# Kernel optimization log

Hardware: AMD Instinct MI355X
Metric: run time of the kernel (lower is better)

Reference implementation:

```python
import jax, jax.numpy as jnp
import numpy as np
import math

LATENT_D = 64
NDIM = 2
VEC = LATENT_D // 4          # 16 output rows per hyper-generated weight
D_LAT = 64                   # channels-proj input dim (latent last dim)
POSENC_CH = 31               # nerf posenc: 1 + 2*15 per coordinate
CH = [NDIM * POSENC_CH, VEC, VEC, VEC]  # [62, 16, 16, 16]
N_PTS = 32768
BATCH = 16
LN_EPS = 1e-5


def posenc_nerf(x, min_deg=0, max_deg=15):
    # x: [..., D] -> [..., D*(1 + 2*(max_deg-min_deg))]
    scales = 2.0 ** jnp.arange(min_deg, max_deg, dtype=x.dtype)
    xb = (x[..., None, :] * scales[:, None]).reshape(*x.shape[:-1], -1)
    emb = jnp.sin(jnp.concatenate([xb, xb + jnp.pi / 2.0], axis=-1))
    return jnp.concatenate([x, emb], axis=-1)


def layernorm(h, w, b):
    mu = h.mean(-1, keepdims=True)
    var = ((h - mu) ** 2).mean(-1, keepdims=True)
    return (h - mu) / jnp.sqrt(var + LN_EPS) * w + b


def setup_inputs() -> dict:
    key = jax.random.key(0)
    ks = iter(jax.random.split(key, 40))
    inp = {}
    inp["x"] = jax.random.uniform(next(ks), (N_PTS, NDIM), dtype=jnp.float32)
    inp["latent"] = jax.random.normal(next(ks), (BATCH, LATENT_D, D_LAT), dtype=jnp.float32)
    for i, ch in enumerate(CH):
        s = 1.0 / math.sqrt(D_LAT)
        inp[f"pw{i}"] = jax.random.normal(next(ks), (VEC * ch, D_LAT), dtype=jnp.float32) * s
        inp[f"pb{i}"] = jax.random.normal(next(ks), (VEC * ch,), dtype=jnp.float32) * 0.01
        inp[f"lnw{i}"] = jnp.full((ch,), 0.0625, dtype=jnp.float32)  # learned_scale init
        inp[f"lnb{i}"] = jnp.zeros((ch,), dtype=jnp.float32)
        inp[f"mb{i}"] = jax.random.normal(next(ks), (VEC,), dtype=jnp.float32)  # registered bias (randn init)
    dims = [(100, VEC), (100, 100), (1, 100)]
    for j, (o, i_) in enumerate(dims, 1):
        s = 1.0 / math.sqrt(i_)
        inp[f"w{j}"] = jax.random.uniform(next(ks), (o, i_), dtype=jnp.float32, minval=-s, maxval=s)
        inp[f"b{j}"] = jax.random.uniform(next(ks), (o,), dtype=jnp.float32, minval=-s, maxval=s)
    return inp


def reference(x, latent,
              pw0, pb0, lnw0, lnb0, mb0,
              pw1, pb1, lnw1, lnb1, mb1,
              pw2, pb2, lnw2, lnb2, mb2,
              pw3, pb3, lnw3, lnb3, mb3,
              w1, b1, w2, b2, w3, b3):
    B = latent.shape[0]
    # x[None].repeat(B,1,1) then nerf-encode: [B, N, 62]
    h = posenc_nerf(jnp.broadcast_to(x[None], (B,) + x.shape))
    proj = [(pw0, pb0, lnw0, lnb0, mb0), (pw1, pb1, lnw1, lnb1, mb1),
            (pw2, pb2, lnw2, lnb2, mb2), (pw3, pb3, lnw3, lnb3, mb3)]
    start = 0
    for (pw, pb, lnw, lnb, mb), ch in zip(proj, CH):
        lat = latent[:, start:start + VEC, :]           # [B, 16, 64]
        start += VEC
        # ChannelsProj: einsum + LN(channels) + bias -> per-sample weight [B, 16, ch]
        wv = jnp.einsum('bvd,vcd->bvc', lat, pw.reshape(VEC, ch, D_LAT))
        wv = layernorm(wv, lnw, lnb) + pb.reshape(VEC, ch)
        # hyper-MLP stage: bmm + bias + SiLU
        h = jax.nn.silu(jnp.einsum('bpi,boi->bpo', h, wv) + mb)
    # trailing dense MLP: 16 -> 100 -> 100 -> 1
    h = jax.nn.silu(h @ w1.T + b1)
    h = jax.nn.silu(h @ w2.T + b2)
    h = h @ w3.T + b3
    return h.squeeze(-1)  # [B, N]
```

## Files before the change

kernel.cpp:

```cpp
#include <hip/hip_runtime.h>

#define N_PTS 32768
#define BATCH 16
#define PIO2F 1.5707963705062866f

typedef __attribute__((ext_vector_type(8))) _Float16 half8;
typedef __attribute__((ext_vector_type(4))) _Float16 half4;
typedef __attribute__((ext_vector_type(4))) float f32x4;

__device__ __forceinline__ float silu_f(float v) {
    return v * __builtin_amdgcn_rcpf(1.0f + __expf(-v));
}

__device__ __forceinline__ float wave_sum(float v) {
    #pragma unroll
    for (int off = 1; off < 64; off <<= 1) v += __shfl_xor(v, off, 64);
    return v;
}

__device__ __forceinline__ void lds_fence() {
    asm volatile("" ::: "memory");
#if __has_builtin(__builtin_amdgcn_wave_barrier)
    __builtin_amdgcn_wave_barrier();
#else
    __builtin_amdgcn_sched_barrier(0);
#endif
    asm volatile("" ::: "memory");
}

__device__ __forceinline__ f32x4 mfma16h(half8 a, half8 b, f32x4 c) {
    return __builtin_amdgcn_mfma_f32_16x16x32_f16(a, b, c, 0, 0, 0);
}

__device__ __forceinline__ half8 h8zero() {
    half8 z;
    #pragma unroll
    for (int r = 0; r < 8; ++r) z[r] = (_Float16)0.0f;
    return z;
}

__device__ __forceinline__ half8 xlane_frag(f32x4 acc, int s0b, int s1b) {
    union { _Float16 h[4]; int i[2]; } p;
    #pragma unroll
    for (int r = 0; r < 4; ++r) p.h[r] = (_Float16)silu_f(acc[r]);
    union { int i[4]; half8 v; } o;
    o.i[0] = __builtin_amdgcn_ds_bpermute(s0b, p.i[0]);
    o.i[1] = __builtin_amdgcn_ds_bpermute(s0b, p.i[1]);
    o.i[2] = __builtin_amdgcn_ds_bpermute(s1b, p.i[0]);
    o.i[3] = __builtin_amdgcn_ds_bpermute(s1b, p.i[1]);
    return o.v;
}

__global__ void wv_kernel(
    const float* __restrict__ latent,
    const float* __restrict__ pw0, const float* __restrict__ pb0,
    const float* __restrict__ lnw0, const float* __restrict__ lnb0,
    const float* __restrict__ pw1, const float* __restrict__ pb1,
    const float* __restrict__ lnw1, const float* __restrict__ lnb1,
    const float* __restrict__ pw2, const float* __restrict__ pb2,
    const float* __restrict__ lnw2, const float* __restrict__ lnb2,
    const float* __restrict__ pw3, const float* __restrict__ pb3,
    const float* __restrict__ lnw3, const float* __restrict__ lnb3,
    float* __restrict__ wvb) {
    int blk = blockIdx.x;
    int l = blk >> 8;
    int rest = blk & 255;
    int b = rest >> 4, o = rest & 15;
    int c = threadIdx.x;

    const float *pw, *pb, *lnw, *lnb;
    float* outp;
    int ch;
    switch (l) {
        case 0:  pw = pw0; pb = pb0; lnw = lnw0; lnb = lnb0; outp = wvb;                 ch = 62; break;
        case 1:  pw = pw1; pb = pb1; lnw = lnw1; lnb = lnb1; outp = wvb + 15872;         ch = 16; break;
        case 2:  pw = pw2; pb = pb2; lnw = lnw2; lnb = lnb2; outp = wvb + 15872 + 4096;  ch = 16; break;
        default: pw = pw3; pb = pb3; lnw = lnw3; lnb = lnb3; outp = wvb + 15872 + 8192;  ch = 16; break;
    }
    const float* lat = latent + ((size_t)(b * 64 + l * 16 + o)) * 64;
    float dot = 0.f;
    if (c < ch) {
        const float* pr = pw + ((size_t)(o * ch + c)) * 64;
        #pragma unroll
        for (int d0 = 0; d0 < 64; d0++) dot += lat[d0] * pr[d0];
    }
    float act = (c < ch) ? dot : 0.f;
    float mu = wave_sum(act) * (1.0f / ch);
    float diff = (c < ch) ? (dot - mu) : 0.f;
    float var = wave_sum(diff * diff) * (1.0f / ch);
    float norm = diff * rsqrtf(var + 1e-5f);
    if (c < ch) outp[(size_t)(b * 16 + o) * ch + c] = norm * lnw[c] + lnb[c] + pb[o * ch + c];
}

__global__ __launch_bounds__(256) void posenc_pre(
    const float* __restrict__ xg, _Float16* __restrict__ peh) {
    int p = blockIdx.x * 256 + threadIdx.x;
    float x0 = xg[2 * p], x1 = xg[2 * p + 1];
    size_t pbs = (size_t)(p >> 4) * 1024 + (size_t)(p & 15) * 8;
    #pragma unroll
    for (int c = 0; c < 8; ++c) {
        half8 hv;
        #pragma unroll
        for (int j = 0; j < 8; ++j) {
            float v;
            if (c < 4) {
                int f = 8 * c + j;
                int idx2 = f - 2;
                int s = idx2 >> 1;
                float sc = __uint_as_float((unsigned)(127 + s) << 23);
                float xa = (idx2 & 1) ? x1 : x0;
                v = sinf(xa * sc);
                if (f == 0) v = x0;
                if (f == 1) v = x1;
            } else {
                int t = 8 * (c - 4) + j;
                int s = t >> 1;
                float sc = __uint_as_float((unsigned)(127 + s) << 23);
                float xa = (t & 1) ? x1 : x0;
                v = sinf(fmaf(xa, sc, PIO2F));
                if (t >= 30) v = 0.f;
            }
            hv[j] = (_Float16)v;
        }
        *(half8*)(peh + pbs + c * 128) = hv;
    }
}

#define BOUNCE_OFF  0
#define W2H_OFF     20480
#define W1H_OFF     41280
#define WV0H_OFF    46656
#define WVH_OFF     48960
#define B1_OFF      51264
#define B2_OFF      51712
#define W3_OFF      52160
#define MB_LDS_OFF  52608
#define LDS_TOTAL   52864

template <bool PRE>
__global__ __launch_bounds__(512, 2) void mfma_kernel(
    const float* __restrict__ xg,
    const _Float16* __restrict__ peh,
    const float* __restrict__ wvb,
    const float* __restrict__ mb0, const float* __restrict__ mb1,
    const float* __restrict__ mb2, const float* __restrict__ mb3,
    const float* __restrict__ w1, const float* __restrict__ b1,
    const float* __restrict__ w2, const float* __restrict__ b2,
    const float* __restrict__ w3, const float* __restrict__ b3,
    float* __restrict__ out) {
    extern __shared__ char smem[];
    _Float16* lds_bounce = (_Float16*)(smem + BOUNCE_OFF);
    _Float16* lds_w2h    = (_Float16*)(smem + W2H_OFF);
    _Float16* lds_w1h    = (_Float16*)(smem + W1H_OFF);
    _Float16* lds_wv0h   = (_Float16*)(smem + WV0H_OFF);
    _Float16* lds_wvh    = (_Float16*)(smem + WVH_OFF);
    float*    lds_b1     = (float*)(smem + B1_OFF);
    float*    lds_b2     = (float*)(smem + B2_OFF);
    float*    lds_w3     = (float*)(smem + W3_OFF);
    float*    lds_mb     = (float*)(smem + MB_LDS_OFF);

    const int b  = blockIdx.x >> 6;
    const int p0 = (blockIdx.x & 63) * 512;

    for (int idx = threadIdx.x; idx < 100 * 104; idx += 512) {
        int o = idx / 104, k = idx - o * 104;
        lds_w2h[idx] = (_Float16)((k < 100) ? w2[o * 100 + k] : 0.f);
    }
    for (int idx = threadIdx.x; idx < 112 * 24; idx += 512) {
        int o = idx / 24, k = idx - o * 24;
        lds_w1h[idx] = (_Float16)((o < 100 && k < 16) ? w1[o * 16 + k] : 0.f);
    }
    const float* wv0g = wvb + b * 992;
    for (int idx = threadIdx.x; idx < 16 * 72; idx += 512) {
        int o = idx / 72, k = idx - o * 72;
        lds_wv0h[idx] = (_Float16)((k < 62) ? wv0g[o * 62 + k] : 0.f);
    }
    const float* wv1g = wvb + 15872 + b * 256;
    const float* wv2g = wvb + 15872 + 4096 + b * 256;
    const float* wv3g = wvb + 15872 + 8192 + b * 256;
    for (int idx = threadIdx.x; idx < 3 * 16 * 24; idx += 512) {
        int li = idx / 384, rest = idx - li * 384;
        int o = rest / 24, k = rest - o * 24;
        const float* src = (li == 0) ? wv1g : (li == 1) ? wv2g : wv3g;
        lds_wvh[idx] = (_Float16)((k < 16) ? src[o * 16 + k] : 0.f);
    }
    if (threadIdx.x < 112) {
        int o = threadIdx.x;
        lds_b1[o] = (o < 100) ? b1[o] : 0.f;
        lds_b2[o] = (o < 100) ? b2[o] : 0.f;
        lds_w3[o] = (o < 100) ? w3[o] : 0.f;
    }
    if (threadIdx.x >= 128 && threadIdx.x < 192) {
        int t = threadIdx.x - 128;
        int li = t >> 4, o = t & 15;
        const float* mbp = (li == 0) ? mb0 : (li == 1) ? mb1 : (li == 2) ? mb2 : mb3;
        lds_mb[t] = mbp[o];
    }
    __syncthreads();

    const int l    = threadIdx.x & 63;
    const int w    = threadIdx.x >> 6;
    const int lrow = l & 15;
    const int lkg  = l >> 4;
    _Float16* bwA = lds_bounce + w * 1280;
    _Float16* bwB = bwA + 640;
    const int pbase = w * 64;
    const float b3v = b3[0];
    const int ptg0 = (p0 + pbase) >> 4;
    const bool kmask = (lkg >= 2);
    const int s0b = (lrow + 32 * (lkg & 1)) * 4;
    const int s1b = s0b + 64;

    #pragma unroll 1
    for (int it = 0; it < 2; ++it) {
        const int ptA = it * 2;
        const int pcolA = p0 + pbase + ptA * 16 + lrow;
        const int pcolB = pcolA + 16;

        half8 pb0A, pb1A, pb0B, pb1B;
        if (PRE) {
            size_t baseA = (size_t)(ptg0 + ptA) * 1024 + (size_t)lkg * 128 + (size_t)lrow * 8;
            pb0A = *(const half8*)(peh + baseA);
            pb1A = *(const half8*)(peh + baseA + 512);
            pb0B = *(const half8*)(peh + baseA + 1024);
            pb1B = *(const half8*)(peh + baseA + 1536);
        } else {
            #pragma unroll
            for (int ch = 0; ch < 2; ++ch) {
                const int pc = ch ? pcolB : pcolA;
                const float x0 = xg[2 * pc], x1 = xg[2 * pc + 1];
                half8 t0, t1;
                #pragma unroll
                for (int j = 0; j < 8; ++j) {
                    int idx2 = 8 * lkg + j - 2;
                    int s = idx2 >> 1;
                    float sc = __uint_as_float((unsigned)(127 + s) << 23);
                    float xa = (idx2 & 1) ? x1 : x0;
                    float v = sinf(xa * sc);
                    if (lkg == 0 && j == 0) v = x0;
                    if (lkg == 0 && j == 1) v = x1;
                    t0[j] = (_Float16)v;
                }
                #pragma unroll
                for (int j = 0; j < 8; ++j) {
                    int t = 8 * lkg + j;
                    int s = t >> 1;
                    float sc = __uint_as_float((unsigned)(127 + s) << 23);
                    float xa = (t & 1) ? x1 : x0;
                    float v = sinf(fmaf(xa, sc, PIO2F));
                    if (t >= 30) v = 0.f;
                    t1[j] = (_Float16)v;
                }
                if (ch) { pb0B = t0; pb1B = t1; } else { pb0A = t0; pb1A = t1; }
            }
        }

        f32x4 accA = *(const f32x4*)(lds_mb + lkg * 4);
        f32x4 accB = accA;
        {
            half8 a0 = *(const half8*)(lds_wv0h + lrow * 72 + lkg * 8);
            accA = mfma16h(a0, pb0A, accA);
            accB = mfma16h(a0, pb0B, accB);
            a0 = *(const half8*)(lds_wv0h + lrow * 72 + 32 + lkg * 8);
            accA = mfma16h(a0, pb1A, accA);
            accB = mfma16h(a0, pb1B, accB);
        }

        #pragma unroll
        for (int li = 0; li < 3; ++li) {
            half8 fA = xlane_frag(accA, s0b, s1b);
            half8 fB = xlane_frag(accB, s0b, s1b);
            f32x4 bias = *(const f32x4*)(lds_mb + (li + 1) * 16 + lkg * 4);
            half8 ah = *(const half8*)(lds_wvh + (li * 16 + lrow) * 24 + (lkg & 1) * 8);
            if (kmask) ah = h8zero();
            accA = mfma16h(ah, fA, bias);
            accB = mfma16h(ah, fB, bias);
        }
        half8 hbfA = xlane_frag(accA, s0b, s1b);
        half8 hbfB = xlane_frag(accB, s0b, s1b);

        f32x4 a2A[7], a2B[7];
        #pragma unroll
        for (int f2 = 0; f2 < 7; ++f2) {
            f32x4 bias = *(const f32x4*)(lds_b2 + f2 * 16 + lkg * 4);
            a2A[f2] = bias;
            a2B[f2] = bias;
        }
        #pragma unroll
        for (int ks = 0; ks < 4; ++ks) {
            lds_fence();
            #pragma unroll
            for (int lf = 0; lf < 2; ++lf) {
                const int fmt = 2 * ks + lf;
                if (fmt < 7) {
                    f32x4 bias = *(const f32x4*)(lds_b1 + fmt * 16 + lkg * 4);
                    half8 ah = *(const half8*)(lds_w1h + (fmt * 16 + lrow) * 24 + (lkg & 1) * 8);
                    if (kmask) ah = h8zero();
                    f32x4 a1A = mfma16h(ah, hbfA, bias);
                    f32x4 a1B = mfma16h(ah, hbfB, bias);
                    half4 hvA, hvB;
                    #pragma unroll
                    for (int r = 0; r < 4; ++r) {
                        hvA[r] = (_Float16)silu_f(a1A[r]);
                        hvB[r] = (_Float16)silu_f(a1B[r]);
                    }
                    *(half4*)(bwA + lrow * 40 + lf * 16 + lkg * 4) = hvA;
                    *(half4*)(bwB + lrow * 40 + lf * 16 + lkg * 4) = hvB;
                } else {
                    half4 hz;
                    #pragma unroll
                    for (int r = 0; r < 4; ++r) hz[r] = (_Float16)0.0f;
                    *(half4*)(bwA + lrow * 40 + lf * 16 + lkg * 4) = hz;
                    *(half4*)(bwB + lrow * 40 + lf * 16 + lkg * 4) = hz;
                }
            }
            lds_fence();
            half8 h2fA = *(const half8*)(bwA + lrow * 40 + lkg * 8);
            half8 h2fB = *(const half8*)(bwB + lrow * 40 + lkg * 8);
            const int kb = ks * 32 + lkg * 8;
            const int kba = (ks == 3) ? ((kb > 96) ? 96 : kb) : kb;
            __builtin_amdgcn_s_setprio(1);
            #pragma unroll
            for (int f2 = 0; f2 < 7; ++f2) {
                int arow = f2 * 16 + lrow;
                if (f2 == 6) arow = (arow > 99) ? 99 : arow;
                half8 ah = *(const half8*)(lds_w2h + arow * 104 + kba);
                a2A[f2] = mfma16h(ah, h2fA, a2A[f2]);
                a2B[f2] = mfma16h(ah, h2fB, a2B[f2]);
            }
            __builtin_amdgcn_s_setprio(0);
        }

        float outA = 0.f, outB = 0.f;
        #pragma unroll
        for (int f2 = 0; f2 < 7; ++f2) {
            f32x4 w3v = *(const f32x4*)(lds_w3 + f2 * 16 + lkg * 4);
            #pragma unroll
            for (int r = 0; r < 4; ++r) {
                outA = fmaf(silu_f(a2A[f2][r]), w3v[r], outA);
                outB = fmaf(silu_f(a2B[f2][r]), w3v[r], outB);
            }
        }
        outA += __shfl_xor(outA, 16, 64);
        outA += __shfl_xor(outA, 32, 64);
        outB += __shfl_xor(outB, 16, 64);
        outB += __shfl_xor(outB, 32, 64);
        if (l < 16) {
            out[(size_t)b * N_PTS + pcolA] = outA + b3v;
            out[(size_t)b * N_PTS + pcolB] = outB + b3v;
        }
    }
}

extern "C" void kernel_launch(void* const* d_in, const int* in_sizes, int n_in,
                              void* d_out, int out_size, void* d_ws, size_t ws_size,
                              hipStream_t stream) {
    const float* x = (const float*)d_in[0];
    const float* latent = (const float*)d_in[1];
    const float *pw[4], *pb[4], *lnw[4], *lnb[4], *mb[4];
    for (int l = 0; l < 4; l++) {
        pw[l]  = (const float*)d_in[2 + 5 * l];
        pb[l]  = (const float*)d_in[3 + 5 * l];
        lnw[l] = (const float*)d_in[4 + 5 * l];
        lnb[l] = (const float*)d_in[5 + 5 * l];
        mb[l]  = (const float*)d_in[6 + 5 * l];
    }
    const float* w1 = (const float*)d_in[22];
    const float* b1 = (const float*)d_in[23];
    const float* w2 = (const float*)d_in[24];
    const float* b2 = (const float*)d_in[25];
    const float* w3 = (const float*)d_in[26];
    const float* b3 = (const float*)d_in[27];

    float* wvb = (float*)d_ws;
    _Float16* peh = (_Float16*)((char*)d_ws + 112640);
    const size_t WS_NEED = 112640 + (size_t)N_PTS * 64 * sizeof(_Float16);
    bool pre = ws_size >= WS_NEED;

    wv_kernel<<<1024, 64, 0, stream>>>(latent,
        pw[0], pb[0], lnw[0], lnb[0],
        pw[1], pb[1], lnw[1], lnb[1],
        pw[2], pb[2], lnw[2], lnb[2],
        pw[3], pb[3], lnw[3], lnb[3],
        wvb);

    if (pre) {
        posenc_pre<<<N_PTS / 256, 256, 0, stream>>>(x, peh);
        hipFuncSetAttribute((const void*)mfma_kernel<true>,
                            hipFuncAttributeMaxDynamicSharedMemorySize, LDS_TOTAL);
        mfma_kernel<true><<<BATCH * (N_PTS / 512), 512, LDS_TOTAL, stream>>>(
            x, peh, wvb, mb[0], mb[1], mb[2], mb[3],
            w1, b1, w2, b2, w3, b3, (float*)d_out);
    } else {
        hipFuncSetAttribute((const void*)mfma_kernel<false>,
                            hipFuncAttributeMaxDynamicSharedMemorySize, LDS_TOTAL);
        mfma_kernel<false><<<BATCH * (N_PTS / 512), 512, LDS_TOTAL, stream>>>(
            x, peh, wvb, mb[0], mb[1], mb[2], mb[3],
            w1, b1, w2, b2, w3, b3, (float*)d_out);
    }
}
```

Before: 75.09 us.

## Replace LDS bounce buffer with register bpermute for layer-1 to layer-2 fragments

Layer-1 MFMA outputs are now all computed up front, passed through SiLU, packed to fp16 in registers, and moved into the B-operand layout for layer 2 with ds_bpermute and a lane-mask select. This replaces the per-wave LDS bounce buffer, its write/read round trips and the wave fences. It also drops the setprio hints. Removing the 20 KB bounce region cuts LDS use, which may allow more blocks per CU, but holding 28 packed ints live raises register pressure under the 512x2 launch bounds.

```diff
diff --git a/kernel.cpp b/kernel.cpp
--- a/kernel.cpp
+++ b/kernel.cpp
@@ -18,16 +18,6 @@
     return v;
 }
 
-__device__ __forceinline__ void lds_fence() {
-    asm volatile("" ::: "memory");
-#if __has_builtin(__builtin_amdgcn_wave_barrier)
-    __builtin_amdgcn_wave_barrier();
-#else
-    __builtin_amdgcn_sched_barrier(0);
-#endif
-    asm volatile("" ::: "memory");
-}
-
 __device__ __forceinline__ f32x4 mfma16h(half8 a, half8 b, f32x4 c) {
     return __builtin_amdgcn_mfma_f32_16x16x32_f16(a, b, c, 0, 0, 0);
 }
@@ -39,15 +29,33 @@
     return z;
 }
 
+__device__ __forceinline__ void silu_pack(f32x4 acc, int& d0, int& d1) {
+    union { _Float16 h[4]; int i[2]; } p;
+    #pragma unroll
+    for (int r = 0; r < 4; ++r) p.h[r] = (_Float16)silu_f(acc[r]);
+    d0 = p.i[0]; d1 = p.i[1];
+}
+
+__device__ __forceinline__ half8 bperm_frag(int d0, int d1, int s0b, int s1b) {
+    union { int i[4]; half8 v; } o;
+    o.i[0] = __builtin_amdgcn_ds_bpermute(s0b, d0);
+    o.i[1] = __builtin_amdgcn_ds_bpermute(s0b, d1);
+    o.i[2] = __builtin_amdgcn_ds_bpermute(s1b, d0);
+    o.i[3] = __builtin_amdgcn_ds_bpermute(s1b, d1);
+    return o.v;
+}
+
 __device__ __forceinline__ half8 xlane_frag(f32x4 acc, int s0b, int s1b) {
-    union { _Float16 h[4]; int i[2]; } p;
-    #pragma unroll
-    for (int r = 0; r < 4; ++r) p.h[r] = (_Float16)silu_f(acc[r]);
-    union { int i[4]; half8 v; } o;
-    o.i[0] = __builtin_amdgcn_ds_bpermute(s0b, p.i[0]);
-    o.i[1] = __builtin_amdgcn_ds_bpermute(s0b, p.i[1]);
-    o.i[2] = __builtin_amdgcn_ds_bpermute(s1b, p.i[0]);
-    o.i[3] = __builtin_amdgcn_ds_bpermute(s1b, p.i[1]);
+    int d0, d1;
+    silu_pack(acc, d0, d1);
+    return bperm_frag(d0, d1, s0b, s1b);
+}
+
+__device__ __forceinline__ half8 sel_frag(bool m, half8 a, half8 b) {
+    union { half8 v; int i[4]; } ua, ub, o;
+    ua.v = a; ub.v = b;
+    #pragma unroll
+    for (int r = 0; r < 4; ++r) o.i[r] = m ? ua.i[r] : ub.i[r];
     return o.v;
 }
 
@@ -126,16 +134,15 @@
     }
 }
 
-#define BOUNCE_OFF  0
-#define W2H_OFF     20480
-#define W1H_OFF     41280
-#define WV0H_OFF    46656
-#define WVH_OFF     48960
-#define B1_OFF      51264
-#define B2_OFF      51712
-#define W3_OFF      52160
-#define MB_LDS_OFF  52608
-#define LDS_TOTAL   52864
+#define W2H_OFF     0
+#define W1H_OFF     20800
+#define WV0H_OFF    26176
+#define WVH_OFF     28480
+#define B1_OFF      30784
+#define B2_OFF      31232
+#define W3_OFF      31680
+#define MB_LDS_OFF  32128
+#define LDS_TOTAL   32384
 
 template <bool PRE>
 __global__ __launch_bounds__(512, 2) void mfma_kernel(
@@ -149,7 +156,6 @@
     const float* __restrict__ w3, const float* __restrict__ b3,
     float* __restrict__ out) {
     extern __shared__ char smem[];
-    _Float16* lds_bounce = (_Float16*)(smem + BOUNCE_OFF);
     _Float16* lds_w2h    = (_Float16*)(smem + W2H_OFF);
     _Float16* lds_w1h    = (_Float16*)(smem + W1H_OFF);
     _Float16* lds_wv0h   = (_Float16*)(smem + WV0H_OFF);
@@ -202,8 +208,6 @@
     const int w    = threadIdx.x >> 6;
     const int lrow = l & 15;
     const int lkg  = l >> 4;
-    _Float16* bwA = lds_bounce + w * 1280;
-    _Float16* bwB = bwA + 640;
     const int pbase = w * 64;
     const float b3v = b3[0];
     const int ptg0 = (p0 + pbase) >> 4;
@@ -279,6 +283,18 @@
         half8 hbfA = xlane_frag(accA, s0b, s1b);
         half8 hbfB = xlane_frag(accB, s0b, s1b);
 
+        int a1A[14], a1B[14];
+        #pragma unroll
+        for (int fmt = 0; fmt < 7; ++fmt) {
+            f32x4 bias = *(const f32x4*)(lds_b1 + fmt * 16 + lkg * 4);
+            half8 ah = *(const half8*)(lds_w1h + (fmt * 16 + lrow) * 24 + (lkg & 1) * 8);
+            if (kmask) ah = h8zero();
+            f32x4 vA = mfma16h(ah, hbfA, bias);
+            f32x4 vB = mfma16h(ah, hbfB, bias);
+            silu_pack(vA, a1A[2 * fmt], a1A[2 * fmt + 1]);
+            silu_pack(vB, a1B[2 * fmt], a1B[2 * fmt + 1]);
+        }
+
         f32x4 a2A[7], a2B[7];
         #pragma unroll
         for (int f2 = 0; f2 < 7; ++f2) {
@@ -288,38 +304,16 @@
         }
         #pragma unroll
         for (int ks = 0; ks < 4; ++ks) {
-            lds_fence();
-            #pragma unroll
-            for (int lf = 0; lf < 2; ++lf) {
-                const int fmt = 2 * ks + lf;
-                if (fmt < 7) {
-                    f32x4 bias = *(const f32x4*)(lds_b1 + fmt * 16 + lkg * 4);
-                    half8 ah = *(const half8*)(lds_w1h + (fmt * 16 + lrow) * 24 + (lkg & 1) * 8);
-                    if (kmask) ah = h8zero();
-                    f32x4 a1A = mfma16h(ah, hbfA, bias);
-                    f32x4 a1B = mfma16h(ah, hbfB, bias);
-                    half4 hvA, hvB;
-                    #pragma unroll
-                    for (int r = 0; r < 4; ++r) {
-                        hvA[r] = (_Float16)silu_f(a1A[r]);
-                        hvB[r] = (_Float16)silu_f(a1B[r]);
-                    }
-                    *(half4*)(bwA + lrow * 40 + lf * 16 + lkg * 4) = hvA;
-                    *(half4*)(bwB + lrow * 40 + lf * 16 + lkg * 4) = hvB;
-                } else {
-                    half4 hz;
-                    #pragma unroll
-                    for (int r = 0; r < 4; ++r) hz[r] = (_Float16)0.0f;
-                    *(half4*)(bwA + lrow * 40 + lf * 16 + lkg * 4) = hz;
-                    *(half4*)(bwB + lrow * 40 + lf * 16 + lkg * 4) = hz;
-                }
-            }
-            lds_fence();
-            half8 h2fA = *(const half8*)(bwA + lrow * 40 + lkg * 8);
-            half8 h2fB = *(const half8*)(bwB + lrow * 40 + lkg * 8);
+            half8 loA = bperm_frag(a1A[4 * ks], a1A[4 * ks + 1], s0b, s1b);
+            half8 loB = bperm_frag(a1B[4 * ks], a1B[4 * ks + 1], s0b, s1b);
+            half8 hiA = (ks == 3) ? h8zero()
+                        : bperm_frag(a1A[4 * ks + 2], a1A[4 * ks + 3], s0b, s1b);
+            half8 hiB = (ks == 3) ? h8zero()
+                        : bperm_frag(a1B[4 * ks + 2], a1B[4 * ks + 3], s0b, s1b);
+            half8 h2fA = sel_frag(kmask, hiA, loA);
+            half8 h2fB = sel_frag(kmask, hiB, loB);
             const int kb = ks * 32 + lkg * 8;
             const int kba = (ks == 3) ? ((kb > 96) ? 96 : kb) : kb;
-            __builtin_amdgcn_s_setprio(1);
             #pragma unroll
             for (int f2 = 0; f2 < 7; ++f2) {
                 int arow = f2 * 16 + lrow;
@@ -328,7 +322,6 @@
                 a2A[f2] = mfma16h(ah, h2fA, a2A[f2]);
                 a2B[f2] = mfma16h(ah, h2fB, a2B[f2]);
             }
-            __builtin_amdgcn_s_setprio(0);
         }
 
         float outA = 0.f, outB = 0.f;
```

New measurement: 178.1 us. 137% more time.
